# Kernel tuning notes

Measured on AMD Instinct MI355X. Metric: run time of the kernel, lower is better.

Reference implementation:

```python
import jax, jax.numpy as jnp
import numpy as np

D_MODEL = 1024
N_HEADS = 16
D_K = D_MODEL // N_HEADS
B, T = 2, 2048
EPS = 1e-6


def _phi(x):
    # elu(x) + 1
    return jax.nn.elu(x) + 1.0


def setup_inputs() -> dict:
    key = jax.random.key(0)
    ks = jax.random.split(key, 5)
    s = 1.0 / np.sqrt(D_MODEL)
    return {
        "x": jax.random.normal(ks[0], (B, T, D_MODEL), jnp.float32),
        "Wq": jax.random.normal(ks[1], (D_MODEL, D_MODEL), jnp.float32) * s,
        "bq": jnp.zeros((D_MODEL,), jnp.float32),
        "Wk": jax.random.normal(ks[2], (D_MODEL, D_MODEL), jnp.float32) * s,
        "bk": jnp.zeros((D_MODEL,), jnp.float32),
        "Wv": jax.random.normal(ks[3], (D_MODEL, D_MODEL), jnp.float32) * s,
        "bv": jnp.zeros((D_MODEL,), jnp.float32),
        "Wo": jax.random.normal(ks[4], (D_MODEL, D_MODEL), jnp.float32) * s,
        "bo": jnp.zeros((D_MODEL,), jnp.float32),
    }


def reference(x, Wq, bq, Wk, bk, Wv, bv, Wo, bo):
    Bv_, Tv_, _ = x.shape
    # projections (torch nn.Linear: x @ W.T + b), split heads -> [B, H, T, d_k]
    def proj(W, b):
        y = x @ W.T + b
        return y.reshape(Bv_, Tv_, N_HEADS, D_K).transpose(0, 2, 1, 3)

    q = _phi(proj(Wq, bq))
    k = _phi(proj(Wk, bk))
    v = proj(Wv, bv)

    # causal linear attention: running kv outer-product and k prefix sums
    kv = jnp.einsum("bhtd,bhte->bhtde", k, v)          # [B,H,T,d_k,d_k]
    kv = jnp.cumsum(kv, axis=2)
    k_cum = jnp.cumsum(k, axis=2)
    out = jnp.einsum("bhtd,bhtde->bhte", q, kv)        # [B,H,T,d_k]
    z = jnp.einsum("bhtd,bhtd->bht", q, k_cum)         # [B,H,T]
    out = out / (z[..., None] + EPS)

    out = out.transpose(0, 2, 1, 3).reshape(Bv_, Tv_, N_HEADS * D_K)
    return out @ Wo.T + bo
```

## Files before the change

### kernel.cpp

```cpp
#include <hip/hip_runtime.h>


typedef float  f32x4   __attribute__((ext_vector_type(4)));
typedef __bf16 bf16x8  __attribute__((ext_vector_type(8)));
typedef short  short8v __attribute__((ext_vector_type(8)));
typedef short  short4v __attribute__((ext_vector_type(4)));

static __device__ __forceinline__ short f2bf(float f) {
    unsigned u = __float_as_uint(f);
    u += 0x7FFFu + ((u >> 16) & 1u);
    return (short)(u >> 16);
}
static __device__ __forceinline__ float bf2f(short s) {
    return __uint_as_float(((unsigned)(unsigned short)s) << 16);
}
static __device__ __forceinline__ float phi(float x) {
    return x > 0.f ? x + 1.f : __expf(x);
}
static __device__ __forceinline__ void gl_lds16(const short* g, short* l) {
    __builtin_amdgcn_global_load_lds(
        (const __attribute__((address_space(1))) void*)g,
        (__attribute__((address_space(3))) void*)l, 16, 0, 0);
}

#define LDT 72
static __device__ __forceinline__ int swz(int row, int col) {
    return row * LDT + (col ^ (row & 56));
}

__global__ __launch_bounds__(256) void convert_bf16(
    const float* __restrict__ x,  const float* __restrict__ Wq,
    const float* __restrict__ Wk, const float* __restrict__ Wv,
    const float* __restrict__ Wo,
    short* __restrict__ xb,  short* __restrict__ Wqb,
    short* __restrict__ Wkb, short* __restrict__ Wvb, short* __restrict__ Wob)
{
    const int blk = blockIdx.x;
    const float* src; short* dst; size_t base;
    if (blk < 2048)      { src = x;  dst = xb;  base = (size_t)blk * 2048; }
    else if (blk < 2560) { src = Wq; dst = Wqb; base = (size_t)(blk - 2048) * 2048; }
    else if (blk < 3072) { src = Wk; dst = Wkb; base = (size_t)(blk - 2560) * 2048; }
    else if (blk < 3584) { src = Wv; dst = Wvb; base = (size_t)(blk - 3072) * 2048; }
    else                 { src = Wo; dst = Wob; base = (size_t)(blk - 3584) * 2048; }
    const size_t o = base + (size_t)threadIdx.x * 8;
    f32x4 v0 = *(const f32x4*)&src[o];
    f32x4 v1 = *(const f32x4*)&src[o + 4];
    short8v s;
#pragma unroll
    for (int m = 0; m < 4; ++m) { s[m] = f2bf(v0[m]); s[m + 4] = f2bf(v1[m]); }
    *(short8v*)&dst[o] = s;
}

__global__ __launch_bounds__(256) void gemm_qkv(
    const short* __restrict__ xb,
    const short* __restrict__ Wqb, const short* __restrict__ Wkb,
    const short* __restrict__ Wvb,
    const float* __restrict__ bq, const float* __restrict__ bk,
    const float* __restrict__ bv,
    short* __restrict__ Qb, short* __restrict__ Kb, short* __restrict__ Vb)
{
    __shared__ short As[128 * 32];
    __shared__ short Bs[128 * 32];
    const int tid = threadIdx.x;
    const int bm = blockIdx.x, bn = blockIdx.y;
    const int wsel = bn >> 3;
    const int n0 = (bn & 7) << 7;
    const short* __restrict__ W    = (wsel == 0) ? Wqb : (wsel == 1) ? Wkb : Wvb;
    const float* __restrict__ bias = (wsel == 0) ? bq  : (wsel == 1) ? bk  : bv;
    short* __restrict__ Ob         = (wsel == 0) ? Qb  : (wsel == 1) ? Kb  : Vb;
    const int m0 = bm << 7;
    const int wave = tid >> 6, lane = tid & 63;
    const int wm = (wave & 1) << 6, wn = (wave >> 1) << 6;
    const int l15 = lane & 15, quad = lane >> 4;

    const int ch0 = wave * 2, ch1 = ch0 + 1;
    const int lrow = lane >> 2;
    const int lcol = (((lane & 3) ^ ((lane >> 3) & 3)) << 3);
    const short* ga0 = xb + (size_t)(m0 + ch0 * 16 + lrow) * 1024 + lcol;
    const short* ga1 = xb + (size_t)(m0 + ch1 * 16 + lrow) * 1024 + lcol;
    const short* gb0 = W  + (size_t)(n0 + ch0 * 16 + lrow) * 1024 + lcol;
    const short* gb1 = W  + (size_t)(n0 + ch1 * 16 + lrow) * 1024 + lcol;
    short* la0 = &As[ch0 * 512];
    short* la1 = &As[ch1 * 512];
    short* lb0 = &Bs[ch0 * 512];
    short* lb1 = &Bs[ch1 * 512];

    const int rslot = (quad ^ ((l15 >> 1) & 3)) << 3;

    f32x4 acc[4][4] = {};
    for (int k0 = 0; k0 < 1024; k0 += 32) {
        __syncthreads();
        gl_lds16(ga0 + k0, la0);
        gl_lds16(ga1 + k0, la1);
        gl_lds16(gb0 + k0, lb0);
        gl_lds16(gb1 + k0, lb1);
        __syncthreads();
        bf16x8 a[4], b[4];
#pragma unroll
        for (int i = 0; i < 4; ++i) a[i] = *(const bf16x8*)&As[(wm + i * 16 + l15) * 32 + rslot];
#pragma unroll
        for (int j = 0; j < 4; ++j) b[j] = *(const bf16x8*)&Bs[(wn + j * 16 + l15) * 32 + rslot];
#pragma unroll
        for (int i = 0; i < 4; ++i)
#pragma unroll
            for (int j = 0; j < 4; ++j)
                acc[i][j] = __builtin_amdgcn_mfma_f32_16x16x32_bf16(a[i], b[j], acc[i][j], 0, 0, 0);
    }

#pragma unroll
    for (int i = 0; i < 4; ++i)
#pragma unroll
        for (int j = 0; j < 4; ++j) {
            const int col = n0 + wn + j * 16 + l15;
            const int h = col >> 6, d = col & 63;
            const float bv_ = bias[col];
            const int row0 = m0 + wm + i * 16 + quad * 4;
            const int b = row0 >> 11, t0 = row0 & 2047;
            const size_t obase = ((size_t)(b * 16 + h) * 2048 + t0) * 64 + d;
#pragma unroll
            for (int r = 0; r < 4; ++r) {
                float v = acc[i][j][r] + bv_;
                if (wsel < 2) v = phi(v);
                Ob[obase + (size_t)r * 64] = f2bf(v);
            }
        }
}

__global__ __launch_bounds__(256) void chunk_sums(
    const short* __restrict__ Kb, const short* __restrict__ Vb,
    short* __restrict__ KVsum, float* __restrict__ ksum)
{
    __shared__ short KT[64 * LDT];
    __shared__ short VT[64 * LDT];
    __shared__ float pS[256];
    const int c = blockIdx.x, bh = blockIdx.y;
    const int tid = threadIdx.x;
    const int w = tid >> 6, lane = tid & 63, l15 = lane & 15, quad = lane >> 4;
    const size_t tilebase = ((size_t)bh * 2048 + c * 64) * 64;

#pragma unroll
    for (int p = 0; p < 2; ++p) {
        const int t = (tid >> 3) + p * 32;
        const int e0 = (tid & 7) << 3;
        const size_t g = tilebase + (size_t)t * 64 + e0;
        short8v kv = *(const short8v*)&Kb[g];
        short8v vv = *(const short8v*)&Vb[g];
#pragma unroll
        for (int jj = 0; jj < 8; ++jj) {
            KT[swz(e0 + jj, t)] = kv[jj];
            VT[swz(e0 + jj, t)] = vv[jj];
        }
    }
    __syncthreads();

    f32x4 acc[4] = {};
#pragma unroll
    for (int k0 = 0; k0 < 64; k0 += 32) {
        const int ra = w * 16 + l15;
        bf16x8 a = *(const bf16x8*)&KT[ra * LDT + ((k0 + quad * 8) ^ (ra & 56))];
#pragma unroll
        for (int tj = 0; tj < 4; ++tj) {
            const int rb = tj * 16 + l15;
            bf16x8 bfr = *(const bf16x8*)&VT[rb * LDT + ((k0 + quad * 8) ^ (rb & 56))];
            acc[tj] = __builtin_amdgcn_mfma_f32_16x16x32_bf16(a, bfr, acc[tj], 0, 0, 0);
        }
    }
    short* __restrict__ outp = KVsum + (((size_t)bh * 32) + c) * 4096;
#pragma unroll
    for (int tj = 0; tj < 4; ++tj)
#pragma unroll
        for (int r = 0; r < 4; ++r)
            outp[(w * 16 + quad * 4 + r) * 64 + tj * 16 + l15] = f2bf(acc[tj][r]);

    {
        const int d = tid & 63, part = tid >> 6;
        short8v k1 = *(const short8v*)&KT[d * LDT + ((part * 16) ^ (d & 56))];
        short8v k2 = *(const short8v*)&KT[d * LDT + ((part * 16 + 8) ^ (d & 56))];
        float s = 0.f;
#pragma unroll
        for (int m = 0; m < 8; ++m) s += bf2f(k1[m]) + bf2f(k2[m]);
        pS[part * 64 + d] = s;
    }
    __syncthreads();
    if (tid < 64)
        ksum[(((size_t)bh * 32) + c) * 64 + tid] =
            pS[tid] + pS[tid + 64] + pS[tid + 128] + pS[tid + 192];
}

__global__ __launch_bounds__(256) void scan_chunks(
    const short* __restrict__ KVsum, const float* __restrict__ ksum,
    short* __restrict__ KVpref, float* __restrict__ kpref)
{
    const int bh = blockIdx.y;
    const int o = blockIdx.x * 256 + threadIdx.x;
    const size_t base = (size_t)bh * 32 * 4096 + o;
    short v[32];
#pragma unroll
    for (int cc = 0; cc < 32; ++cc) v[cc] = KVsum[base + (size_t)cc * 4096];
    float run = 0.f;
#pragma unroll
    for (int cc = 0; cc < 32; ++cc) {
        KVpref[base + (size_t)cc * 4096] = f2bf(run);
        run += bf2f(v[cc]);
    }
    if (blockIdx.x == 0 && threadIdx.x < 64) {
        float vals[32];
        const size_t kb = (size_t)bh * 32 * 64 + threadIdx.x;
#pragma unroll
        for (int cc = 0; cc < 32; ++cc) vals[cc] = ksum[kb + (size_t)cc * 64];
        float r2 = 0.f;
#pragma unroll
        for (int cc = 0; cc < 32; ++cc) { kpref[kb + (size_t)cc * 64] = r2; r2 += vals[cc]; }
    }
}

__global__ __launch_bounds__(256) void attn_chunk(
    const short* __restrict__ Qb, const short* __restrict__ Kb,
    const short* __restrict__ Vb, const short* __restrict__ KVpref,
    const float* __restrict__ kpref, short* __restrict__ attnb)
{
    __shared__ short Qs[64 * LDT];
    __shared__ short KS[64 * LDT];
    __shared__ short VT[64 * LDT];
    __shared__ short KVT[64 * LDT];
    const int c = blockIdx.x, bh = blockIdx.y;
    const int b = bh >> 4, h = bh & 15;
    const int tid = threadIdx.x;
    const int w = tid >> 6, lane = tid & 63, l15 = lane & 15, quad = lane >> 4;
    const size_t tilebase = ((size_t)bh * 2048 + c * 64) * 64;
    const short* __restrict__ KVc = KVpref + (((size_t)bh * 32) + c) * 4096;

#pragma unroll
    for (int p = 0; p < 2; ++p) {
        const int t = (tid >> 3) + p * 32;
        const int e0 = (tid & 7) << 3;
        const size_t g = tilebase + (size_t)t * 64 + e0;
        *(short8v*)&Qs[t * LDT + e0] = *(const short8v*)&Qb[g];
        *(short8v*)&KS[t * LDT + e0] = *(const short8v*)&Kb[g];
        short8v vv = *(const short8v*)&Vb[g];
        short8v pv = *(const short8v*)&KVc[t * 64 + e0];
#pragma unroll
        for (int jj = 0; jj < 8; ++jj) {
            VT[swz(e0 + jj, t)]  = vv[jj];
            KVT[swz(e0 + jj, t)] = pv[jj];
        }
    }
    __syncthreads();

    f32x4 sacc[4] = {};
#pragma unroll
    for (int k0 = 0; k0 < 64; k0 += 32) {
        bf16x8 a = *(const bf16x8*)&Qs[(w * 16 + l15) * LDT + k0 + quad * 8];
#pragma unroll
        for (int tj = 0; tj < 4; ++tj) {
            bf16x8 bfr = *(const bf16x8*)&KS[(tj * 16 + l15) * LDT + k0 + quad * 8];
            sacc[tj] = __builtin_amdgcn_mfma_f32_16x16x32_bf16(a, bfr, sacc[tj], 0, 0, 0);
        }
    }

    f32x4 kp4 = *(const f32x4*)&kpref[(((size_t)bh * 32) + c) * 64 + l15 * 4];
    float zinv[4];
#pragma unroll
    for (int r = 0; r < 4; ++r) {
        const int i = w * 16 + quad * 4 + r;
        float p = 0.f;
#pragma unroll
        for (int tj = 0; tj < 4; ++tj)
            if (tj * 16 + l15 <= i) p += sacc[tj][r];
        short4v q4 = *(const short4v*)&Qs[i * LDT + l15 * 4];
#pragma unroll
        for (int m = 0; m < 4; ++m) p += bf2f(q4[m]) * kp4[m];
        p += __shfl_xor(p, 1);
        p += __shfl_xor(p, 2);
        p += __shfl_xor(p, 4);
        p += __shfl_xor(p, 8);
        zinv[r] = 1.f / (p + 1e-6f);
    }

    __syncthreads();
#pragma unroll
    for (int tj = 0; tj < 4; ++tj)
#pragma unroll
        for (int r = 0; r < 4; ++r) {
            const int i = w * 16 + quad * 4 + r;
            const int j = tj * 16 + l15;
            KS[i * LDT + j] = f2bf(j <= i ? sacc[tj][r] : 0.f);
        }

    f32x4 oacc[4] = {};
#pragma unroll
    for (int k0 = 0; k0 < 64; k0 += 32) {
        bf16x8 a1 = *(const bf16x8*)&KS[(w * 16 + l15) * LDT + k0 + quad * 8];
        bf16x8 a2 = *(const bf16x8*)&Qs[(w * 16 + l15) * LDT + k0 + quad * 8];
#pragma unroll
        for (int tj = 0; tj < 4; ++tj) {
            const int rb = tj * 16 + l15;
            bf16x8 b1 = *(const bf16x8*)&VT[rb * LDT + ((k0 + quad * 8) ^ (rb & 56))];
            bf16x8 b2 = *(const bf16x8*)&KVT[rb * LDT + ((k0 + quad * 8) ^ (rb & 56))];
            oacc[tj] = __builtin_amdgcn_mfma_f32_16x16x32_bf16(a1, b1, oacc[tj], 0, 0, 0);
            oacc[tj] = __builtin_amdgcn_mfma_f32_16x16x32_bf16(a2, b2, oacc[tj], 0, 0, 0);
        }
    }
    const size_t arowbase = (size_t)b * 2048 + c * 64;
#pragma unroll
    for (int tj = 0; tj < 4; ++tj)
#pragma unroll
        for (int r = 0; r < 4; ++r) {
            const int i = w * 16 + quad * 4 + r;
            const int e = tj * 16 + l15;
            attnb[(arowbase + i) * 1024 + h * 64 + e] = f2bf(oacc[tj][r] * zinv[r]);
        }
}

__global__ __launch_bounds__(256) void gemm_out(
    const short* __restrict__ attnb, const short* __restrict__ Wob,
    const float* __restrict__ bo, float* __restrict__ outp)
{
    __shared__ short As[128 * 32];
    __shared__ short Bs[64 * 32];
    const int tid = threadIdx.x;
    const int bm = blockIdx.x, bn = blockIdx.y;
    const int m0 = bm << 7, n0 = bn << 6;
    const int wave = tid >> 6, lane = tid & 63;
    const int wm = (wave & 1) << 6, wn = (wave >> 1) << 5;
    const int l15 = lane & 15, quad = lane >> 4;

    const int lrow = lane >> 2;
    const int lcol = (((lane & 3) ^ ((lane >> 3) & 3)) << 3);
    const short* gp[3]; short* lp[3];
#pragma unroll
    for (int cc = 0; cc < 3; ++cc) {
        const int ch = wave * 3 + cc;
        if (ch < 8) {
            gp[cc] = attnb + (size_t)(m0 + ch * 16 + lrow) * 1024 + lcol;
            lp[cc] = &As[ch * 512];
        } else {
            gp[cc] = Wob + (size_t)(n0 + (ch - 8) * 16 + lrow) * 1024 + lcol;
            lp[cc] = &Bs[(ch - 8) * 512];
        }
    }
    const int rslot = (quad ^ ((l15 >> 1) & 3)) << 3;

    f32x4 acc[4][2] = {};
    for (int k0 = 0; k0 < 1024; k0 += 32) {
        __syncthreads();
        gl_lds16(gp[0] + k0, lp[0]);
        gl_lds16(gp[1] + k0, lp[1]);
        gl_lds16(gp[2] + k0, lp[2]);
        __syncthreads();
        bf16x8 a[4], b[2];
#pragma unroll
        for (int i = 0; i < 4; ++i) a[i] = *(const bf16x8*)&As[(wm + i * 16 + l15) * 32 + rslot];
#pragma unroll
        for (int j = 0; j < 2; ++j) b[j] = *(const bf16x8*)&Bs[(wn + j * 16 + l15) * 32 + rslot];
#pragma unroll
        for (int i = 0; i < 4; ++i)
#pragma unroll
            for (int j = 0; j < 2; ++j)
                acc[i][j] = __builtin_amdgcn_mfma_f32_16x16x32_bf16(a[i], b[j], acc[i][j], 0, 0, 0);
    }

#pragma unroll
    for (int i = 0; i < 4; ++i)
#pragma unroll
        for (int j = 0; j < 2; ++j) {
            const int col = n0 + wn + j * 16 + l15;
            const float bv_ = bo[col];
#pragma unroll
            for (int r = 0; r < 4; ++r) {
                const int row = m0 + wm + i * 16 + quad * 4 + r;
                outp[(size_t)row * 1024 + col] = acc[i][j][r] + bv_;
            }
        }
}

extern "C" void kernel_launch(void* const* d_in, const int* in_sizes, int n_in,
                              void* d_out, int out_size, void* d_ws, size_t ws_size,
                              hipStream_t stream)
{
    const float* x  = (const float*)d_in[0];
    const float* Wq = (const float*)d_in[1];
    const float* bq = (const float*)d_in[2];
    const float* Wk = (const float*)d_in[3];
    const float* bk = (const float*)d_in[4];
    const float* Wv = (const float*)d_in[5];
    const float* bv = (const float*)d_in[6];
    const float* Wo = (const float*)d_in[7];
    const float* bo = (const float*)d_in[8];

    char* ws = (char*)d_ws;
    short* xb     = (short*)(ws + 0);
    short* Wqb    = (short*)(ws + 8388608);
    short* Wkb    = (short*)(ws + 10485760);
    short* Wvb    = (short*)(ws + 12582912);
    short* Wob    = (short*)(ws + 14680064);
    short* Qb     = (short*)(ws + 16777216);
    short* Kb     = (short*)(ws + 25165824);
    short* Vb     = (short*)(ws + 33554432);
    short* KVsum  = (short*)(ws + 41943040);
    short* KVpref = (short*)(ws + 50331648);
    short* attnb  = (short*)(ws + 58720256);
    float* ksum   = (float*)(ws + 67108864);
    float* kpref  = (float*)(ws + 67371008);
    float* outp   = (float*)d_out;

    convert_bf16<<<4096, 256, 0, stream>>>(x, Wq, Wk, Wv, Wo, xb, Wqb, Wkb, Wvb, Wob);
    gemm_qkv   <<<dim3(32, 24), 256, 0, stream>>>(xb, Wqb, Wkb, Wvb, bq, bk, bv, Qb, Kb, Vb);
    chunk_sums <<<dim3(32, 32), 256, 0, stream>>>(Kb, Vb, KVsum, ksum);
    scan_chunks<<<dim3(16, 32), 256, 0, stream>>>(KVsum, ksum, KVpref, kpref);
    attn_chunk <<<dim3(32, 32), 256, 0, stream>>>(Qb, Kb, Vb, KVpref, kpref, attnb);
    gemm_out   <<<dim3(32, 16), 256, 0, stream>>>(attnb, Wob, bo, outp);
}
```

Before: 158.0 us.

## Double-buffer LDS tiles in QKV and output GEMMs to overlap loads with MFMA

Both GEMM kernels now keep two LDS buffers and issue the async global-to-LDS loads for the next K-slice before running the MFMAs on the current one. The goal is to hide global memory latency behind compute instead of stalling on each 32-wide K step. In exchange the kernels use twice as much shared memory, which may reduce occupancy, and the explicit vmcnt(0) waits plus barriers may still serialize part of the overlap.

New measurement: 160.7 us. About the same (+1.7%).

```diff
diff --git a/kernel.cpp b/kernel.cpp
--- a/kernel.cpp
+++ b/kernel.cpp
@@ -59,8 +59,8 @@
     const float* __restrict__ bv,
     short* __restrict__ Qb, short* __restrict__ Kb, short* __restrict__ Vb)
 {
-    __shared__ short As[128 * 32];
-    __shared__ short Bs[128 * 32];
+    __shared__ short As[2][128 * 32];
+    __shared__ short Bs[2][128 * 32];
     const int tid = threadIdx.x;
     const int bm = blockIdx.x, bn = blockIdx.y;
     const int wsel = bn >> 3;
@@ -80,32 +80,52 @@
     const short* ga1 = xb + (size_t)(m0 + ch1 * 16 + lrow) * 1024 + lcol;
     const short* gb0 = W  + (size_t)(n0 + ch0 * 16 + lrow) * 1024 + lcol;
     const short* gb1 = W  + (size_t)(n0 + ch1 * 16 + lrow) * 1024 + lcol;
-    short* la0 = &As[ch0 * 512];
-    short* la1 = &As[ch1 * 512];
-    short* lb0 = &Bs[ch0 * 512];
-    short* lb1 = &Bs[ch1 * 512];
+    short* la0[2] = { &As[0][ch0 * 512], &As[1][ch0 * 512] };
+    short* la1[2] = { &As[0][ch1 * 512], &As[1][ch1 * 512] };
+    short* lb0[2] = { &Bs[0][ch0 * 512], &Bs[1][ch0 * 512] };
+    short* lb1[2] = { &Bs[0][ch1 * 512], &Bs[1][ch1 * 512] };
 
     const int rslot = (quad ^ ((l15 >> 1) & 3)) << 3;
 
+#define QKV_STAGE(K, BUF)                    \
+    do {                                     \
+        gl_lds16(ga0 + (K), la0[BUF]);       \
+        gl_lds16(ga1 + (K), la1[BUF]);       \
+        gl_lds16(gb0 + (K), lb0[BUF]);       \
+        gl_lds16(gb1 + (K), lb1[BUF]);       \
+    } while (0)
+
+#define QKV_COMPUTE(BUF)                                                              \
+    do {                                                                              \
+        bf16x8 a[4], b[4];                                                            \
+        _Pragma("unroll")                                                             \
+        for (int i = 0; i < 4; ++i)                                                   \
+            a[i] = *(const bf16x8*)&As[BUF][(wm + i * 16 + l15) * 32 + rslot];        \
+        _Pragma("unroll")                                                             \
+        for (int j = 0; j < 4; ++j)                                                   \
+            b[j] = *(const bf16x8*)&Bs[BUF][(wn + j * 16 + l15) * 32 + rslot];        \
+        _Pragma("unroll")                                                             \
+        for (int i = 0; i < 4; ++i)                                                   \
+            _Pragma("unroll")                                                         \
+            for (int j = 0; j < 4; ++j)                                               \
+                acc[i][j] = __builtin_amdgcn_mfma_f32_16x16x32_bf16(a[i], b[j],       \
+                                                                   acc[i][j], 0, 0, 0); \
+    } while (0)
+
     f32x4 acc[4][4] = {};
-    for (int k0 = 0; k0 < 1024; k0 += 32) {
+    QKV_STAGE(0, 0);
+    for (int k0 = 0; k0 < 1024; k0 += 64) {
+        asm volatile("s_waitcnt vmcnt(0)" ::: "memory");
         __syncthreads();
-        gl_lds16(ga0 + k0, la0);
-        gl_lds16(ga1 + k0, la1);
-        gl_lds16(gb0 + k0, lb0);
-        gl_lds16(gb1 + k0, lb1);
+        QKV_STAGE(k0 + 32, 1);
+        QKV_COMPUTE(0);
+        asm volatile("s_waitcnt vmcnt(0)" ::: "memory");
         __syncthreads();
-        bf16x8 a[4], b[4];
-#pragma unroll
-        for (int i = 0; i < 4; ++i) a[i] = *(const bf16x8*)&As[(wm + i * 16 + l15) * 32 + rslot];
-#pragma unroll
-        for (int j = 0; j < 4; ++j) b[j] = *(const bf16x8*)&Bs[(wn + j * 16 + l15) * 32 + rslot];
-#pragma unroll
-        for (int i = 0; i < 4; ++i)
-#pragma unroll
-            for (int j = 0; j < 4; ++j)
-                acc[i][j] = __builtin_amdgcn_mfma_f32_16x16x32_bf16(a[i], b[j], acc[i][j], 0, 0, 0);
-    }
+        if (k0 + 64 < 1024) QKV_STAGE(k0 + 64, 0);
+        QKV_COMPUTE(1);
+    }
+#undef QKV_STAGE
+#undef QKV_COMPUTE
 
 #pragma unroll
     for (int i = 0; i < 4; ++i)
@@ -316,8 +336,8 @@
     const short* __restrict__ attnb, const short* __restrict__ Wob,
     const float* __restrict__ bo, float* __restrict__ outp)
 {
-    __shared__ short As[128 * 32];
-    __shared__ short Bs[64 * 32];
+    __shared__ short As[2][128 * 32];
+    __shared__ short Bs[2][64 * 32];
     const int tid = threadIdx.x;
     const int bm = blockIdx.x, bn = blockIdx.y;
     const int m0 = bm << 7, n0 = bn << 6;
@@ -327,38 +347,60 @@
 
     const int lrow = lane >> 2;
     const int lcol = (((lane & 3) ^ ((lane >> 3) & 3)) << 3);
-    const short* gp[3]; short* lp[3];
+    const short* gp[3]; short* lp[2][3];
 #pragma unroll
     for (int cc = 0; cc < 3; ++cc) {
         const int ch = wave * 3 + cc;
         if (ch < 8) {
             gp[cc] = attnb + (size_t)(m0 + ch * 16 + lrow) * 1024 + lcol;
-            lp[cc] = &As[ch * 512];
+            lp[0][cc] = &As[0][ch * 512];
+            lp[1][cc] = &As[1][ch * 512];
         } else {
             gp[cc] = Wob + (size_t)(n0 + (ch - 8) * 16 + lrow) * 1024 + lcol;
-            lp[cc] = &Bs[(ch - 8) * 512];
+            lp[0][cc] = &Bs[0][(ch - 8) * 512];
+            lp[1][cc] = &Bs[1][(ch - 8) * 512];
         }
     }
     const int rslot = (quad ^ ((l15 >> 1) & 3)) << 3;
 
+#define OUT_STAGE(K, BUF)                     \
+    do {                                      \
+        gl_lds16(gp[0] + (K), lp[BUF][0]);    \
+        gl_lds16(gp[1] + (K), lp[BUF][1]);    \
+        gl_lds16(gp[2] + (K), lp[BUF][2]);    \
+    } while (0)
+
+#define OUT_COMPUTE(BUF)                                                              \
+    do {                                                                              \
+        bf16x8 a[4], b[2];                                                            \
+        _Pragma("unroll")                                                             \
+        for (int i = 0; i < 4; ++i)                                                   \
+            a[i] = *(const bf16x8*)&As[BUF][(wm + i * 16 + l15) * 32 + rslot];        \
+        _Pragma("unroll")                                                             \
+        for (int j = 0; j < 2; ++j)                                                   \
+            b[j] = *(const bf16x8*)&Bs[BUF][(wn + j * 16 + l15) * 32 + rslot];        \
+        _Pragma("unroll")                                                             \
+        for (int i = 0; i < 4; ++i)                                                   \
+            _Pragma("unroll")                                                         \
+            for (int j = 0; j < 2; ++j)                                               \
+                acc[i][j] = __builtin_amdgcn_mfma_f32_16x16x32_bf16(a[i], b[j],       \
+                                                                   acc[i][j], 0, 0, 0); \
+    } while (0)
+
     f32x4 acc[4][2] = {};
-    for (int k0 = 0; k0 < 1024; k0 += 32) {
+    OUT_STAGE(0, 0);
+    for (int k0 = 0; k0 < 1024; k0 += 64) {
+        asm volatile("s_waitcnt vmcnt(0)" ::: "memory");
         __syncthreads();
-        gl_lds16(gp[0] + k0, lp[0]);
-        gl_lds16(gp[1] + k0, lp[1]);
-        gl_lds16(gp[2] + k0, lp[2]);
+        OUT_STAGE(k0 + 32, 1);
+        OUT_COMPUTE(0);
+        asm volatile("s_waitcnt vmcnt(0)" ::: "memory");
         __syncthreads();
-        bf16x8 a[4], b[2];
-#pragma unroll
-        for (int i = 0; i < 4; ++i) a[i] = *(const bf16x8*)&As[(wm + i * 16 + l15) * 32 + rslot];
-#pragma unroll
-        for (int j = 0; j < 2; ++j) b[j] = *(const bf16x8*)&Bs[(wn + j * 16 + l15) * 32 + rslot];
-#pragma unroll
-        for (int i = 0; i < 4; ++i)
-#pragma unroll
-            for (int j = 0; j < 2; ++j)
-                acc[i][j] = __builtin_amdgcn_mfma_f32_16x16x32_bf16(a[i], b[j], acc[i][j], 0, 0, 0);
-    }
+        if (k0 + 64 < 1024) OUT_STAGE(k0 + 64, 0);
+        OUT_COMPUTE(1);
+    }
+#undef OUT_STAGE
+#undef OUT_COMPUTE
 
 #pragma unroll
     for (int i = 0; i < 4; ++i)
```
